# Kernel tuning notes

Measured on AMD Instinct MI355X. Metric: run time of the kernel, lower is better.

Reference implementation:

```python
import jax, jax.numpy as jnp
import numpy as np

B, S, D, F, O = 4, 2048, 1024, 4096, 1024
E, NS, K = 4, 2, 2  # routed experts, shared experts, topk


def setup_inputs() -> dict:
    key = jax.random.key(0)
    ks = jax.random.split(key, 6)
    def w(k, shape, fan_in):
        return jax.random.normal(k, shape, jnp.float32) * (fan_in ** -0.5)
    return {
        "x": jax.random.normal(ks[0], (B, S, D), jnp.float32),
        "gate_w": w(ks[1], (D, E), D),
        "gate_b": jnp.zeros((E,), jnp.float32),
        "sw1": w(ks[2], (NS, D, F), D),  # shared experts, first linear
        "sb1": jnp.zeros((NS, F), jnp.float32),
        "sw2": w(ks[3], (NS, F, O), F),
        "sb2": jnp.zeros((NS, O), jnp.float32),
        "rw1": w(ks[4], (E, D, F), D),   # routed experts, first linear
        "rb1": jnp.zeros((E, F), jnp.float32),
        "rw2": w(ks[5], (E, F, O), F),
        "rb2": jnp.zeros((E, O), jnp.float32),
    }


def reference(x, gate_w, gate_b, sw1, sb1, sw2, sb2, rw1, rb1, rw2, rb2):
    # Gating (eval mode: no noise)
    weights = jax.nn.softmax(x @ gate_w + gate_b, axis=-1)      # [B,S,E]
    topk_w, topk_i = jax.lax.top_k(weights, K)                  # [B,S,K]

    # Shared experts: average of NS expert MLPs
    sh = jax.nn.relu(jnp.einsum('bsd,ndf->bsnf', x, sw1) + sb1)
    shared = (jnp.einsum('bsnf,nfo->bsno', sh, sw2) + sb2).sum(axis=2) / NS  # [B,S,O]

    # Routed experts: every expert applied densely, then one-hot-select topk.
    # Original computes expert(expanded_x) where expanded_x repeats x K times;
    # the result is identical per copy, so compute once per expert and gather.
    rh = jax.nn.relu(jnp.einsum('bsd,edf->bsef', x, rw1) + rb1)  # [B,S,E,F]
    eo = jnp.einsum('bsef,efo->bseo', rh, rw2) + rb2             # [B,S,E,O]
    gathered = jnp.take_along_axis(eo, topk_i[..., None], axis=2)  # [B,S,K,O]
    routed = (gathered * topk_w[..., None]).sum(axis=2)          # [B,S,O]

    return shared + routed
```

## Files before the change

### kernel.cpp

```cpp
#include <hip/hip_runtime.h>

typedef __bf16 bf16_t;
typedef __bf16 bf16x8 __attribute__((ext_vector_type(8)));
typedef float f32x4 __attribute__((ext_vector_type(4)));

constexpr int Tn = 4 * 2048;
constexpr int Dd = 1024;
constexpr int Ff = 4096;
constexpr int Oo = 1024;
constexpr int NEXP = 6;

__device__ __forceinline__ float ldin(const void* p, size_t i, int isf32) {
    return isf32 ? ((const float*)p)[i] : (float)((const bf16_t*)p)[i];
}

__global__ void detect_kernel(const unsigned int* __restrict__ xw, int* __restrict__ flag) {
    __shared__ int cnt;
    if (threadIdx.x == 0) cnt = 0;
    __syncthreads();
    int c = 0;
    for (int i = threadIdx.x; i < 16384; i += 256) {
        unsigned w = xw[i];
        if (((w >> 7) & 0xFFu) == 0xFFu) ++c;
    }
    atomicAdd(&cnt, c);
    __syncthreads();
    if (threadIdx.x == 0) flag[0] = (cnt >= 4) ? 1 : 0;
}

__global__ void cvt_x_kernel(const void* __restrict__ x, const int* __restrict__ flag,
                             bf16_t* __restrict__ xb) {
    int f = flag[0];
    size_t i = (size_t)blockIdx.x * 256 + threadIdx.x;
    xb[i] = (bf16_t)ldin(x, i, f);
}

__global__ void cvt_transpose_kernel(const void* __restrict__ src, size_t eofs,
                                     const int* __restrict__ flag,
                                     bf16_t* __restrict__ dst, int R, int C) {
    __shared__ bf16_t tile[32][33];
    int f = flag[0];
    int c0 = blockIdx.x * 32, r0 = blockIdx.y * 32;
    int tx = threadIdx.x, ty = threadIdx.y;
    #pragma unroll
    for (int i = 0; i < 32; i += 8)
        tile[ty + i][tx] = (bf16_t)ldin(src, eofs + (size_t)(r0 + ty + i) * C + c0 + tx, f);
    __syncthreads();
    #pragma unroll
    for (int i = 0; i < 32; i += 8)
        dst[(size_t)(c0 + ty + i) * R + r0 + tx] = tile[tx][ty + i];
}

__global__ void gate_kernel(const void* __restrict__ x, const void* __restrict__ gw,
                            const void* __restrict__ gb, const int* __restrict__ flag,
                            float* __restrict__ coef) {
    int f = flag[0];
    int t = blockIdx.x;
    int lane = threadIdx.x;
    float a0 = 0.f, a1 = 0.f, a2 = 0.f, a3 = 0.f;
    for (int d = lane; d < Dd; d += 64) {
        float xv = ldin(x, (size_t)t * Dd + d, f);
        a0 += xv * ldin(gw, (size_t)d * 4 + 0, f);
        a1 += xv * ldin(gw, (size_t)d * 4 + 1, f);
        a2 += xv * ldin(gw, (size_t)d * 4 + 2, f);
        a3 += xv * ldin(gw, (size_t)d * 4 + 3, f);
    }
    #pragma unroll
    for (int off = 32; off; off >>= 1) {
        a0 += __shfl_xor(a0, off);
        a1 += __shfl_xor(a1, off);
        a2 += __shfl_xor(a2, off);
        a3 += __shfl_xor(a3, off);
    }
    if (lane == 0) {
        float l[4] = {a0 + ldin(gb, 0, f), a1 + ldin(gb, 1, f),
                      a2 + ldin(gb, 2, f), a3 + ldin(gb, 3, f)};
        float mx = fmaxf(fmaxf(l[0], l[1]), fmaxf(l[2], l[3]));
        float e[4], s = 0.f;
        #pragma unroll
        for (int i = 0; i < 4; ++i) { e[i] = expf(l[i] - mx); s += e[i]; }
        float w[4];
        #pragma unroll
        for (int i = 0; i < 4; ++i) w[i] = e[i] / s;
        int i0 = 0;
        for (int i = 1; i < 4; ++i) if (w[i] > w[i0]) i0 = i;
        int i1 = -1;
        for (int i = 0; i < 4; ++i) { if (i == i0) continue; if (i1 < 0 || w[i] > w[i1]) i1 = i; }
        float c[8] = {0.5f, 0.5f, 0.f, 0.f, 0.f, 0.f, 0.f, 0.f};
        c[2 + i0] = w[i0];
        c[2 + i1] = w[i1];
        float* dst = coef + (size_t)t * 8;
        #pragma unroll
        for (int k = 0; k < 8; ++k) dst[k] = c[k];
    }
}

__global__ void init_acc_kernel(const float* __restrict__ coef, const void* __restrict__ sb2,
                                const void* __restrict__ rb2, const int* __restrict__ flag,
                                float* __restrict__ acc) {
    int f = flag[0];
    size_t idx = (size_t)blockIdx.x * 256 + threadIdx.x;
    int t = (int)(idx >> 10);
    int o = (int)(idx & 1023);
    const float* c = coef + (size_t)t * 8;
    float v = c[0] * ldin(sb2, o, f) + c[1] * ldin(sb2, Oo + o, f)
            + c[2] * ldin(rb2, o, f) + c[3] * ldin(rb2, Oo + o, f)
            + c[4] * ldin(rb2, 2 * Oo + o, f) + c[5] * ldin(rb2, 3 * Oo + o, f);
    acc[idx] = v;
}

__global__ void convert_kernel(const float* __restrict__ acc, const int* __restrict__ flag,
                               void* __restrict__ out) {
    int f = flag[0];
    size_t idx = (size_t)blockIdx.x * 256 + threadIdx.x;
    float v = acc[idx];
    if (v != v) v = 333.0f;
    if (f) ((float*)out)[idx] = v;
    else   ((bf16_t*)out)[idx] = (bf16_t)v;
}

template <int MODE>
__launch_bounds__(256, 2)
__global__ void gemm_kernel(const bf16_t* __restrict__ A, const bf16_t* __restrict__ Bt,
                            int M, int N, int K,
                            const void* __restrict__ bias, size_t b1_e,
                            const int* __restrict__ flag,
                            const float* __restrict__ coef,
                            bf16_t* __restrict__ obf, float* __restrict__ oacc) {
    constexpr int BM = 128, BN = 128, BK = 64;
    __shared__ __align__(16) bf16_t Al[BM * BK];
    __shared__ __align__(16) bf16_t Bl[BN * BK];

    const int tid = threadIdx.x;
    const int lane = tid & 63;
    const int wave = tid >> 6;
    const int wm = wave & 1, wn = wave >> 1;
    const int bm = blockIdx.x * BM;
    const int bn = blockIdx.y * BN;
    const int l15 = lane & 15;
    const int l4 = lane >> 4;
    const int r7 = l15 & 7;

    f32x4 acc[4][4] = {};

    for (int k0 = 0; k0 < K; k0 += BK) {
        #pragma unroll
        for (int it = 0; it < 4; ++it) {
            int q = it * 256 + tid;
            int row = q >> 3, c8s = q & 7;
            int k8 = c8s ^ (row & 7);
            const bf16_t* g = A + (size_t)(bm + row) * K + k0 + k8 * 8;
            __builtin_amdgcn_global_load_lds(
                (const __attribute__((address_space(1))) unsigned int*)g,
                (__attribute__((address_space(3))) unsigned int*)(&Al[q * 8]), 16, 0, 0);
        }
        #pragma unroll
        for (int it = 0; it < 4; ++it) {
            int q = it * 256 + tid;
            int row = q >> 3, c8s = q & 7;
            int k8 = c8s ^ (row & 7);
            const bf16_t* g = Bt + (size_t)(bn + row) * K + k0 + k8 * 8;
            __builtin_amdgcn_global_load_lds(
                (const __attribute__((address_space(1))) unsigned int*)g,
                (__attribute__((address_space(3))) unsigned int*)(&Bl[q * 8]), 16, 0, 0);
        }
        __syncthreads();
        #pragma unroll
        for (int kk = 0; kk < BK; kk += 32) {
            const int k8f = l4 + (kk >> 3);
            const int c8s = (k8f ^ r7) * 8;
            bf16x8 af[4], bfv[4];
            #pragma unroll
            for (int i = 0; i < 4; ++i)
                af[i] = *(const bf16x8*)&Al[(wm * 64 + i * 16 + l15) * BK + c8s];
            #pragma unroll
            for (int j = 0; j < 4; ++j)
                bfv[j] = *(const bf16x8*)&Bl[(wn * 64 + j * 16 + l15) * BK + c8s];
            #pragma unroll
            for (int i = 0; i < 4; ++i)
                #pragma unroll
                for (int j = 0; j < 4; ++j)
                    acc[i][j] = __builtin_amdgcn_mfma_f32_16x16x32_bf16(af[i], bfv[j], acc[i][j], 0, 0, 0);
        }
        __syncthreads();
    }

    if (MODE == 1) {
        int isf32 = flag[0];
        float bz[4];
        #pragma unroll
        for (int j = 0; j < 4; ++j)
            bz[j] = ldin(bias, b1_e + (size_t)(bn + wn * 64 + j * 16 + l15), isf32);
        #pragma unroll
        for (int i = 0; i < 4; ++i) {
            #pragma unroll
            for (int r = 0; r < 4; ++r) {
                int m = bm + wm * 64 + i * 16 + l4 * 4 + r;
                float cf = coef[(size_t)m * 8];
                #pragma unroll
                for (int j = 0; j < 4; ++j) {
                    float v = acc[i][j][r] + bz[j];
                    v = fmaxf(v, 0.f) * cf;
                    obf[(size_t)m * N + bn + wn * 64 + j * 16 + l15] = (bf16_t)v;
                }
            }
        }
    } else {
        #pragma unroll
        for (int i = 0; i < 4; ++i) {
            #pragma unroll
            for (int r = 0; r < 4; ++r) {
                int m = bm + wm * 64 + i * 16 + l4 * 4 + r;
                float* orow = oacc + (size_t)m * N + bn + wn * 64 + l15;
                #pragma unroll
                for (int j = 0; j < 4; ++j)
                    orow[j * 16] += acc[i][j][r];
            }
        }
    }
}

extern "C" void kernel_launch(void* const* d_in, const int* in_sizes, int n_in,
                              void* d_out, int out_size, void* d_ws, size_t ws_size,
                              hipStream_t stream) {
    const void* x      = d_in[0];
    const void* gate_w = d_in[1];
    const void* gate_b = d_in[2];
    const void* sw1    = d_in[3];
    const void* sb1    = d_in[4];
    const void* sw2    = d_in[5];
    const void* sb2    = d_in[6];
    const void* rw1    = d_in[7];
    const void* rb1    = d_in[8];
    const void* rw2    = d_in[9];
    const void* rb2    = d_in[10];

    char* ws = (char*)d_ws;
    int* flag = (int*)ws;
    size_t off = 256;
    bf16_t* W1T = (bf16_t*)(ws + off); off += (size_t)Ff * Dd * sizeof(bf16_t);
    bf16_t* W2T = (bf16_t*)(ws + off); off += (size_t)Oo * Ff * sizeof(bf16_t);
    bf16_t* xb  = (bf16_t*)(ws + off); off += (size_t)Tn * Dd * sizeof(bf16_t);
    float* coef = (float*)(ws + off);  off += (size_t)Tn * 8 * sizeof(float);
    float* accb = (float*)(ws + off);  off += (size_t)Tn * Oo * sizeof(float);
    bf16_t* Hs  = (bf16_t*)(ws + off);
    size_t rem = (ws_size > off) ? (ws_size - off) : 0;
    long tcap = (long)(rem / ((size_t)Ff * sizeof(bf16_t)));
    int Tc = (int)((tcap / 128) * 128);
    if (Tc < 128) Tc = 128;
    if (Tc > Tn) Tc = Tn;

    detect_kernel<<<1, 256, 0, stream>>>((const unsigned int*)x, flag);
    cvt_x_kernel<<<(Tn * Dd) / 256, 256, 0, stream>>>(x, flag, xb);
    gate_kernel<<<Tn, 64, 0, stream>>>(x, gate_w, gate_b, flag, coef);
    init_acc_kernel<<<(Tn * Oo) / 256, 256, 0, stream>>>(coef, sb2, rb2, flag, accb);

    dim3 tb(32, 8);
    for (int j = 0; j < NEXP; ++j) {
        const void* w1 = (j < 2) ? sw1 : rw1;
        const void* w2 = (j < 2) ? sw2 : rw2;
        const void* b1 = (j < 2) ? sb1 : rb1;
        int je = (j < 2) ? j : (j - 2);
        size_t w1_e = (size_t)je * Dd * Ff;
        size_t w2_e = (size_t)je * Ff * Oo;
        size_t b1_e = (size_t)je * Ff;

        cvt_transpose_kernel<<<dim3(Ff / 32, Dd / 32), tb, 0, stream>>>(w1, w1_e, flag, W1T, Dd, Ff);
        cvt_transpose_kernel<<<dim3(Oo / 32, Ff / 32), tb, 0, stream>>>(w2, w2_e, flag, W2T, Ff, Oo);

        for (int tok0 = 0; tok0 < Tn; tok0 += Tc) {
            int tc = (Tn - tok0 < Tc) ? (Tn - tok0) : Tc;
            gemm_kernel<1><<<dim3(tc / 128, Ff / 128), 256, 0, stream>>>(
                xb + (size_t)tok0 * Dd, W1T, tc, Ff, Dd,
                b1, b1_e, flag, coef + (size_t)tok0 * 8 + j, Hs, nullptr);
            gemm_kernel<2><<<dim3(tc / 128, Oo / 128), 256, 0, stream>>>(
                Hs, W2T, tc, Oo, Ff, nullptr, 0, flag, nullptr, nullptr, accb + (size_t)tok0 * Oo);
        }
    }

    convert_kernel<<<(Tn * Oo) / 256, 256, 0, stream>>>(accb, flag, d_out);
}
```

Before: 1.237 ms.

## Route tokens to selected experts via gathered index lists instead of dense compute

The gate kernel now builds per-expert token lists with atomics, and the GEMMs gather rows by token index, so each routed expert only processes its assigned tokens. Blocks past the padded count exit early, and the second GEMM scatters results back by token. This avoids the dense computation over all tokens for every routed expert, which is multiplied by a zero coefficient for the unselected ones. The two weight transpose launches are also merged into one. The cost is indirect, gathered loads and scattered writes, plus atomic ordering that makes the token order nondeterministic.

After: 1.337 ms. 1.08x slower.

```diff
diff --git a/kernel.cpp b/kernel.cpp
--- a/kernel.cpp
+++ b/kernel.cpp
@@ -28,6 +28,17 @@
     if (threadIdx.x == 0) flag[0] = (cnt >= 4) ? 1 : 0;
 }
 
+__global__ void setup_lists_kernel(int* __restrict__ cnt, int* __restrict__ tokidx) {
+    int i = blockIdx.x * 256 + threadIdx.x;
+    tokidx[0 * Tn + i] = i;
+    tokidx[1 * Tn + i] = i;
+    tokidx[2 * Tn + i] = 0;
+    tokidx[3 * Tn + i] = 0;
+    tokidx[4 * Tn + i] = 0;
+    tokidx[5 * Tn + i] = 0;
+    if (i < 6) cnt[i] = (i < 2) ? Tn : 0;
+}
+
 __global__ void cvt_x_kernel(const void* __restrict__ x, const int* __restrict__ flag,
                              bf16_t* __restrict__ xb) {
     int f = flag[0];
@@ -35,25 +46,38 @@
     xb[i] = (bf16_t)ldin(x, i, f);
 }
 
-__global__ void cvt_transpose_kernel(const void* __restrict__ src, size_t eofs,
-                                     const int* __restrict__ flag,
-                                     bf16_t* __restrict__ dst, int R, int C) {
+__global__ void cvt_transpose2_kernel(const void* __restrict__ w1, size_t e1,
+                                      const void* __restrict__ w2, size_t e2,
+                                      const int* __restrict__ flag,
+                                      bf16_t* __restrict__ W1T, bf16_t* __restrict__ W2T) {
     __shared__ bf16_t tile[32][33];
     int f = flag[0];
-    int c0 = blockIdx.x * 32, r0 = blockIdx.y * 32;
+    int b = blockIdx.x;
+    const void* src; size_t eofs; bf16_t* dst; int Rr, Cc, bx, by;
+    constexpr int NB1 = (Ff / 32) * (Dd / 32);
+    if (b < NB1) {
+        src = w1; eofs = e1; dst = W1T; Rr = Dd; Cc = Ff;
+        bx = b % (Ff / 32); by = b / (Ff / 32);
+    } else {
+        b -= NB1;
+        src = w2; eofs = e2; dst = W2T; Rr = Ff; Cc = Oo;
+        bx = b % (Oo / 32); by = b / (Oo / 32);
+    }
+    int c0 = bx * 32, r0 = by * 32;
     int tx = threadIdx.x, ty = threadIdx.y;
     #pragma unroll
     for (int i = 0; i < 32; i += 8)
-        tile[ty + i][tx] = (bf16_t)ldin(src, eofs + (size_t)(r0 + ty + i) * C + c0 + tx, f);
+        tile[ty + i][tx] = (bf16_t)ldin(src, eofs + (size_t)(r0 + ty + i) * Cc + c0 + tx, f);
     __syncthreads();
     #pragma unroll
     for (int i = 0; i < 32; i += 8)
-        dst[(size_t)(c0 + ty + i) * R + r0 + tx] = tile[tx][ty + i];
+        dst[(size_t)(c0 + ty + i) * Rr + r0 + tx] = tile[tx][ty + i];
 }
 
 __global__ void gate_kernel(const void* __restrict__ x, const void* __restrict__ gw,
                             const void* __restrict__ gb, const int* __restrict__ flag,
-                            float* __restrict__ coef) {
+                            float* __restrict__ coef, int* __restrict__ cnt,
+                            int* __restrict__ tokidx) {
     int f = flag[0];
     int t = blockIdx.x;
     int lane = threadIdx.x;
@@ -92,6 +116,10 @@
         float* dst = coef + (size_t)t * 8;
         #pragma unroll
         for (int k = 0; k < 8; ++k) dst[k] = c[k];
+        int p0 = atomicAdd(&cnt[2 + i0], 1);
+        tokidx[(size_t)(2 + i0) * Tn + p0] = t;
+        int p1 = atomicAdd(&cnt[2 + i1], 1);
+        tokidx[(size_t)(2 + i1) * Tn + p1] = t;
     }
 }
 
@@ -122,20 +150,26 @@
 template <int MODE>
 __launch_bounds__(256, 2)
 __global__ void gemm_kernel(const bf16_t* __restrict__ A, const bf16_t* __restrict__ Bt,
-                            int M, int N, int K,
+                            int N, int K,
+                            const int* __restrict__ tokidx_e, const int* __restrict__ cntp,
+                            int ofs,
                             const void* __restrict__ bias, size_t b1_e,
                             const int* __restrict__ flag,
-                            const float* __restrict__ coef,
+                            const float* __restrict__ coefc,
                             bf16_t* __restrict__ obf, float* __restrict__ oacc) {
     constexpr int BM = 128, BN = 128, BK = 64;
     __shared__ __align__(16) bf16_t Al[BM * BK];
     __shared__ __align__(16) bf16_t Bl[BN * BK];
 
+    const int Mj = cntp[0];
+    const int Mpad = (Mj + 127) & ~127;
+    const int bm = blockIdx.x * BM;
+    if (ofs + bm >= Mpad) return;
+
     const int tid = threadIdx.x;
     const int lane = tid & 63;
     const int wave = tid >> 6;
     const int wm = wave & 1, wn = wave >> 1;
-    const int bm = blockIdx.x * BM;
     const int bn = blockIdx.y * BN;
     const int l15 = lane & 15;
     const int l4 = lane >> 4;
@@ -149,7 +183,13 @@
             int q = it * 256 + tid;
             int row = q >> 3, c8s = q & 7;
             int k8 = c8s ^ (row & 7);
-            const bf16_t* g = A + (size_t)(bm + row) * K + k0 + k8 * 8;
+            const bf16_t* g;
+            if (MODE == 1) {
+                int tok = tokidx_e[ofs + bm + row];
+                g = A + (size_t)tok * K + k0 + k8 * 8;
+            } else {
+                g = A + (size_t)(bm + row) * K + k0 + k8 * 8;
+            }
             __builtin_amdgcn_global_load_lds(
                 (const __attribute__((address_space(1))) unsigned int*)g,
                 (__attribute__((address_space(3))) unsigned int*)(&Al[q * 8]), 16, 0, 0);
@@ -195,13 +235,15 @@
         for (int i = 0; i < 4; ++i) {
             #pragma unroll
             for (int r = 0; r < 4; ++r) {
-                int m = bm + wm * 64 + i * 16 + l4 * 4 + r;
-                float cf = coef[(size_t)m * 8];
+                int lm = bm + wm * 64 + i * 16 + l4 * 4 + r;
+                int gm = ofs + lm;
+                int tok = tokidx_e[gm];
+                float cf = (gm < Mj) ? coefc[(size_t)tok * 8] : 0.f;
                 #pragma unroll
                 for (int j = 0; j < 4; ++j) {
                     float v = acc[i][j][r] + bz[j];
                     v = fmaxf(v, 0.f) * cf;
-                    obf[(size_t)m * N + bn + wn * 64 + j * 16 + l15] = (bf16_t)v;
+                    obf[(size_t)lm * N + bn + wn * 64 + j * 16 + l15] = (bf16_t)v;
                 }
             }
         }
@@ -210,11 +252,15 @@
         for (int i = 0; i < 4; ++i) {
             #pragma unroll
             for (int r = 0; r < 4; ++r) {
-                int m = bm + wm * 64 + i * 16 + l4 * 4 + r;
-                float* orow = oacc + (size_t)m * N + bn + wn * 64 + l15;
-                #pragma unroll
-                for (int j = 0; j < 4; ++j)
-                    orow[j * 16] += acc[i][j][r];
+                int lm = bm + wm * 64 + i * 16 + l4 * 4 + r;
+                int gm = ofs + lm;
+                if (gm < Mj) {
+                    int tok = tokidx_e[gm];
+                    float* orow = oacc + (size_t)tok * N + bn + wn * 64 + l15;
+                    #pragma unroll
+                    for (int j = 0; j < 4; ++j)
+                        orow[j * 16] += acc[i][j][r];
+                }
             }
         }
     }
@@ -236,8 +282,10 @@
     const void* rb2    = d_in[10];
 
     char* ws = (char*)d_ws;
-    int* flag = (int*)ws;
+    int* cnt  = (int*)ws;
+    int* flag = (int*)(ws + 64);
     size_t off = 256;
+    int* tokidx = (int*)(ws + off);    off += (size_t)NEXP * Tn * sizeof(int);
     bf16_t* W1T = (bf16_t*)(ws + off); off += (size_t)Ff * Dd * sizeof(bf16_t);
     bf16_t* W2T = (bf16_t*)(ws + off); off += (size_t)Oo * Ff * sizeof(bf16_t);
     bf16_t* xb  = (bf16_t*)(ws + off); off += (size_t)Tn * Dd * sizeof(bf16_t);
@@ -251,30 +299,33 @@
     if (Tc > Tn) Tc = Tn;
 
     detect_kernel<<<1, 256, 0, stream>>>((const unsigned int*)x, flag);
+    setup_lists_kernel<<<Tn / 256, 256, 0, stream>>>(cnt, tokidx);
     cvt_x_kernel<<<(Tn * Dd) / 256, 256, 0, stream>>>(x, flag, xb);
-    gate_kernel<<<Tn, 64, 0, stream>>>(x, gate_w, gate_b, flag, coef);
+    gate_kernel<<<Tn, 64, 0, stream>>>(x, gate_w, gate_b, flag, coef, cnt, tokidx);
     init_acc_kernel<<<(Tn * Oo) / 256, 256, 0, stream>>>(coef, sb2, rb2, flag, accb);
 
-    dim3 tb(32, 8);
-    for (int j = 0; j < NEXP; ++j) {
-        const void* w1 = (j < 2) ? sw1 : rw1;
-        const void* w2 = (j < 2) ? sw2 : rw2;
-        const void* b1 = (j < 2) ? sb1 : rb1;
-        int je = (j < 2) ? j : (j - 2);
+    constexpr int NTB = (Ff / 32) * (Dd / 32) + (Oo / 32) * (Ff / 32);
+    for (int e = 0; e < NEXP; ++e) {
+        const void* w1 = (e < 2) ? sw1 : rw1;
+        const void* w2 = (e < 2) ? sw2 : rw2;
+        const void* b1 = (e < 2) ? sb1 : rb1;
+        int je = (e < 2) ? e : (e - 2);
         size_t w1_e = (size_t)je * Dd * Ff;
         size_t w2_e = (size_t)je * Ff * Oo;
         size_t b1_e = (size_t)je * Ff;
 
-        cvt_transpose_kernel<<<dim3(Ff / 32, Dd / 32), tb, 0, stream>>>(w1, w1_e, flag, W1T, Dd, Ff);
-        cvt_transpose_kernel<<<dim3(Oo / 32, Ff / 32), tb, 0, stream>>>(w2, w2_e, flag, W2T, Ff, Oo);
-
-        for (int tok0 = 0; tok0 < Tn; tok0 += Tc) {
-            int tc = (Tn - tok0 < Tc) ? (Tn - tok0) : Tc;
+        cvt_transpose2_kernel<<<NTB, dim3(32, 8), 0, stream>>>(w1, w1_e, w2, w2_e, flag, W1T, W2T);
+
+        const int* tokidx_e = tokidx + (size_t)e * Tn;
+        const int* cntp = cnt + e;
+        for (int ofs = 0; ofs < Tn; ofs += Tc) {
+            int tc = (Tn - ofs < Tc) ? (Tn - ofs) : Tc;
             gemm_kernel<1><<<dim3(tc / 128, Ff / 128), 256, 0, stream>>>(
-                xb + (size_t)tok0 * Dd, W1T, tc, Ff, Dd,
-                b1, b1_e, flag, coef + (size_t)tok0 * 8 + j, Hs, nullptr);
+                xb, W1T, Ff, Dd, tokidx_e, cntp, ofs,
+                b1, b1_e, flag, coef + e, Hs, nullptr);
             gemm_kernel<2><<<dim3(tc / 128, Oo / 128), 256, 0, stream>>>(
-                Hs, W2T, tc, Oo, Ff, nullptr, 0, flag, nullptr, nullptr, accb + (size_t)tok0 * Oo);
+                Hs, W2T, Oo, Ff, tokidx_e, cntp, ofs,
+                nullptr, 0, flag, nullptr, nullptr, accb);
         }
     }
 
```
